# Kernel tuning notes

Hardware: AMD Instinct MI355X
Metric: run time of the kernel (lower is better)

Reference implementation:

```python
import jax, jax.numpy as jnp
import numpy as np

B, S, D = 2, 1024, 1024
N_HEADS = 16
R = 128
M = 8
N_NEURONS = 256


def group_gate(gate, n_basis):
    # gate: [B,S,N] -> [B,S,M], sum over consecutive groups, then normalize
    b, s, n = gate.shape
    gs = n // n_basis  # exact by construction (256/8)
    g = gate.reshape(b, s, n_basis, gs).sum(axis=-1)
    return g / (g.sum(axis=-1, keepdims=True) + 1e-8)


def feature_fn(x, neurons, weights):
    # x:[B,S,D], neurons:[M,D,R], weights:[B,S,M] -> h:[B,S,R]
    all_h = jnp.einsum('bsd,mdr->bsmr', x, neurons)
    return jnp.einsum('bsmr,bsm->bsr', all_h, weights)


def restore_fn(h, neurons, weights):
    # h:[B,S,R], neurons:[M,R,D], weights:[B,S,M] -> [B,S,D]
    pre = jnp.einsum('bsr,bsm->bsmr', h, weights)
    return jnp.einsum('bsmr,mrd->bsd', pre, neurons)


def setup_inputs() -> dict:
    key = jax.random.key(0)
    ks = jax.random.split(key, 9)
    sc = 0.02
    return {
        'x': jax.random.normal(ks[0], (B, S, D), jnp.float32),
        'qk_f': jax.random.normal(ks[1], (M, D, R), jnp.float32) * sc,
        'qk_r': jax.random.normal(ks[2], (M, R, D), jnp.float32) * sc,
        'v_f': jax.random.normal(ks[3], (M, D, R), jnp.float32) * sc,
        'v_r': jax.random.normal(ks[4], (M, R, D), jnp.float32) * sc,
        'Wg_q': jax.random.normal(ks[5], (D, N_NEURONS), jnp.float32) * sc,
        'Wg_k': jax.random.normal(ks[6], (D, N_NEURONS), jnp.float32) * sc,
        'Wg_v': jax.random.normal(ks[7], (D, N_NEURONS), jnp.float32) * sc,
        'W_O': jax.random.normal(ks[8], (D, D), jnp.float32) * sc,
    }


def reference(x, qk_f, qk_r, v_f, v_r, Wg_q, Wg_k, Wg_v, W_O):
    # Router gates (softmax over neuron dim), then grouped per basis
    g_Q = jax.nn.softmax(jnp.einsum('bsd,dn->bsn', x, Wg_q), axis=-1)
    g_K = jax.nn.softmax(jnp.einsum('bsd,dn->bsn', x, Wg_k), axis=-1)
    g_V = jax.nn.softmax(jnp.einsum('bsd,dn->bsn', x, Wg_v), axis=-1)
    gQ_b = group_gate(g_Q, M)
    gK_b = group_gate(g_K, M)
    gV_b = group_gate(g_V, M)

    Q = restore_fn(feature_fn(x, qk_f, gQ_b), qk_r, gQ_b)
    K = restore_fn(feature_fn(x, qk_f, gK_b), qk_r, gK_b)
    V = restore_fn(feature_fn(x, v_f, gV_b), v_r, gV_b)

    d_head = D // N_HEADS
    Q = Q.reshape(B, S, N_HEADS, d_head).transpose(0, 2, 1, 3)
    K = K.reshape(B, S, N_HEADS, d_head).transpose(0, 2, 1, 3)
    V = V.reshape(B, S, N_HEADS, d_head).transpose(0, 2, 1, 3)

    scale = jnp.sqrt(jnp.float32(d_head))
    scores = jnp.einsum('bhsd,bhtd->bhst', Q, K) / scale
    causal = jnp.tril(jnp.ones((S, S), dtype=jnp.bool_))
    scores = jnp.where(causal, scores, jnp.finfo(scores.dtype).min)
    attn_w = jax.nn.softmax(scores, axis=-1)
    out = jnp.einsum('bhst,bhtd->bhsd', attn_w, V)
    out = out.transpose(0, 2, 1, 3).reshape(B, S, D)
    out = jnp.einsum('bsd,de->bse', out, W_O)
    return out
```

## Files before the change

### kernel.cpp

```cpp
#include <hip/hip_runtime.h>
#include <hip/hip_bf16.h>

#define BB 2
#define SS 1024
#define DD 1024
#define NH 16
#define DH 64
#define MM 8
#define RR 128
#define NN 256
#define NT (BB*SS)

using bf16 = __hip_bfloat16;

typedef __attribute__((ext_vector_type(8))) short short8;
typedef __attribute__((ext_vector_type(4))) short short4v;
typedef __attribute__((ext_vector_type(4))) float f32x4;

#define EXP2F(x) __builtin_amdgcn_exp2f(x)

#define GLD16(g, l) __builtin_amdgcn_global_load_lds( \
    (const __attribute__((address_space(1))) void*)(g), \
    (__attribute__((address_space(3))) void*)(l), 16, 0, 0)

__device__ __forceinline__ short8 lds_load8(const short* p) {
    short4v a = *(const short4v*)p;
    short4v b = *(const short4v*)(p + 4);
    short8 r;
    r[0] = a[0]; r[1] = a[1]; r[2] = a[2]; r[3] = a[3];
    r[4] = b[0]; r[5] = b[1]; r[6] = b[2]; r[7] = b[3];
    return r;
}

template <int NR>
__device__ __forceinline__ void stage_tile(const bf16* __restrict__ src, int k0,
                                           bf16* lds, int wave, int lane) {
#pragma unroll
    for (int i = 0; i < NR / 32; ++i) {
        const int L = i * 256 + wave * 64 + lane;
        const int row = L >> 3;
        const int gch = (L & 7) ^ ((row >> 1) & 7);
        GLD16(src + (size_t)row * DD + k0 + gch * 8, &lds[(i * 256 + wave * 64) * 8]);
    }
}

__device__ __forceinline__ short8 fragld(const bf16* lds, int rc, int kk, int quad) {
    int slot = (kk * 4 + quad) ^ ((rc >> 1) & 7);
    return *(const short8*)&((const short*)lds)[(rc * 8 + slot) * 8];
}

__device__ __forceinline__ void gemm64_pipe2(
    const bf16* __restrict__ A, const bf16* __restrict__ Bt, bf16* __restrict__ C,
    int Nz, int m0, int n0, bf16* As, bf16* Bs,
    int wave, int lane, int quad, int l15) {
    const int wr = wave >> 1, wc = wave & 1;
    f32x4 acc[2][4];
#pragma unroll
    for (int i = 0; i < 2; ++i)
#pragma unroll
        for (int j = 0; j < 4; ++j) acc[i][j] = (f32x4)0.f;

    const bf16* Ab = A + (size_t)m0 * DD;
    const bf16* Bb = Bt + (size_t)n0 * DD;

    stage_tile<64>(Ab, 0, As, wave, lane);
    stage_tile<128>(Bb, 0, Bs, wave, lane);
    stage_tile<64>(Ab, 64, As + 4096, wave, lane);
    stage_tile<128>(Bb, 64, Bs + 8192, wave, lane);

    int cur = 0;
    for (int it = 0; it < 16; ++it) {
        const int k0 = it * 64;
        int nxt = cur + 2; if (nxt >= 3) nxt -= 3;
        if (it < 14) {
            stage_tile<64>(Ab, k0 + 128, As + nxt * 4096, wave, lane);
            stage_tile<128>(Bb, k0 + 128, Bs + nxt * 8192, wave, lane);
            asm volatile("s_waitcnt vmcnt(12)" ::: "memory");
        } else if (it == 14) {
            asm volatile("s_waitcnt vmcnt(6)" ::: "memory");
        } else {
            asm volatile("s_waitcnt vmcnt(0)" ::: "memory");
        }
        __builtin_amdgcn_s_barrier();

        const bf16* Asc = As + cur * 4096;
        const bf16* Bsc = Bs + cur * 8192;
#pragma unroll
        for (int kk = 0; kk < 2; ++kk) {
            short8 aF[2], bF[4];
#pragma unroll
            for (int bi = 0; bi < 2; ++bi) aF[bi] = fragld(Asc, wr * 32 + bi * 16 + l15, kk, quad);
#pragma unroll
            for (int bj = 0; bj < 4; ++bj) bF[bj] = fragld(Bsc, wc * 64 + bj * 16 + l15, kk, quad);
#pragma unroll
            for (int bi = 0; bi < 2; ++bi)
#pragma unroll
                for (int bj = 0; bj < 4; ++bj)
                    acc[bi][bj] = __builtin_amdgcn_mfma_f32_16x16x32_bf16(aF[bi], bF[bj], acc[bi][bj], 0, 0, 0);
        }
        __builtin_amdgcn_s_barrier();
        cur = cur + 1; if (cur == 3) cur = 0;
    }

#pragma unroll
    for (int bi = 0; bi < 2; ++bi)
#pragma unroll
        for (int bj = 0; bj < 4; ++bj)
#pragma unroll
            for (int r = 0; r < 4; ++r) {
                int row = m0 + wr * 32 + bi * 16 + quad * 4 + r;
                int col = n0 + wc * 64 + bj * 16 + l15;
                C[(size_t)row * Nz + col] = __float2bfloat16(acc[bi][bj][r]);
            }
}

struct ProjArgs {
    const bf16 *xb, *f0, *f1, *wg;
    bf16 *allh0, *allh1, *lg;
    const float* csrc[3];
    bf16* cdst[3];
};

__global__ __launch_bounds__(256, 2) void mfma_proj(ProjArgs P) {
    __shared__ __align__(16) char smem[73728];
    const int bidx = blockIdx.x;
    const int tid = threadIdx.x;

    if (bidx >= 704) {
        float (*tile)[33] = (float(*)[33])smem;
        const int cb = bidx - 704;
        const int j = cb >> 10;
        const int t = cb & 1023;
        const int kb = t >> 5, rb = t & 31;
        const int tx = tid & 31, ty0 = tid >> 5;
        const float* s = P.csrc[j] + ((size_t)(kb * 32) * 1024) + rb * 32 + tx;
#pragma unroll
        for (int p = 0; p < 4; ++p)
            tile[ty0 + p * 8][tx] = s[(size_t)(ty0 + p * 8) * 1024];
        __syncthreads();
        bf16* dd = P.cdst[j] + ((size_t)(rb * 32) * 1024) + kb * 32 + tx;
#pragma unroll
        for (int p = 0; p < 4; ++p)
            dd[(size_t)(ty0 + p * 8) * 1024] = __float2bfloat16(tile[tx][ty0 + p * 8]);
        return;
    }

    bf16* As = (bf16*)smem;
    bf16* Bs = As + 3 * 64 * 64;
    const int wave = tid >> 6, lane = tid & 63;
    const int quad = lane >> 4, l15 = lane & 15;
    const int wk = (bidx & 7) * 88 + (bidx >> 3);
    if (wk < 512) {
        const int z = wk >> 8;
        const int r = wk & 255;
        gemm64_pipe2(P.xb, z ? P.f1 : P.f0, z ? P.allh1 : P.allh0, 1024,
                     (r >> 3) * 64, (r & 7) * 128, As, Bs, wave, lane, quad, l15);
    } else {
        const int r = wk - 512;
        gemm64_pipe2(P.xb, P.wg, P.lg, 768, (r / 6) * 64, (r % 6) * 128,
                     As, Bs, wave, lane, quad, l15);
    }
}

struct RestZ {
    const bf16* A[3];
    const bf16* Bt[3];
    bf16* C[3];
};

__global__ __launch_bounds__(256, 2) void mfma_restore(RestZ R) {
    __shared__ __align__(16) char smem[73728];
    bf16* As = (bf16*)smem;
    bf16* Bs = As + 3 * 64 * 64;
    const int tid = threadIdx.x;
    const int wave = tid >> 6, lane = tid & 63;
    const int quad = lane >> 4, l15 = lane & 15;
    const int wk = (blockIdx.x & 7) * 96 + (blockIdx.x >> 3);
    const int z = wk >> 8;
    const int r = wk & 255;
    gemm64_pipe2(R.A[z], R.Bt[z], R.C[z], DD, (r >> 3) * 64, (r & 7) * 128,
                 As, Bs, wave, lane, quad, l15);
}

__global__ __launch_bounds__(256, 3) void mfma_wo(
    const bf16* __restrict__ A, const bf16* __restrict__ Bt, float* __restrict__ C) {
    __shared__ __align__(16) bf16 As[3 * 64 * 64];
    __shared__ __align__(16) bf16 Bs[3 * 64 * 64];
    const int tid = threadIdx.x;
    const int wave = tid >> 6, lane = tid & 63;
    const int quad = lane >> 4, l15 = lane & 15;
    const int wr = wave >> 1, wc = wave & 1;
    const int wk = (blockIdx.x & 7) * 64 + (blockIdx.x >> 3);
    const int m0 = (wk >> 4) * 64, n0 = (wk & 15) * 64;

    f32x4 acc[2][2];
#pragma unroll
    for (int i = 0; i < 2; ++i)
#pragma unroll
        for (int j = 0; j < 2; ++j) acc[i][j] = (f32x4)0.f;

    const bf16* Ab = A + (size_t)m0 * DD;
    const bf16* Bb = Bt + (size_t)n0 * DD;

    stage_tile<64>(Ab, 0, As, wave, lane);
    stage_tile<64>(Bb, 0, Bs, wave, lane);
    stage_tile<64>(Ab, 64, As + 4096, wave, lane);
    stage_tile<64>(Bb, 64, Bs + 4096, wave, lane);

    int cur = 0;
    for (int it = 0; it < 16; ++it) {
        const int k0 = it * 64;
        int nxt = cur + 2; if (nxt >= 3) nxt -= 3;
        if (it < 14) {
            stage_tile<64>(Ab, k0 + 128, As + nxt * 4096, wave, lane);
            stage_tile<64>(Bb, k0 + 128, Bs + nxt * 4096, wave, lane);
            asm volatile("s_waitcnt vmcnt(8)" ::: "memory");
        } else if (it == 14) {
            asm volatile("s_waitcnt vmcnt(4)" ::: "memory");
        } else {
            asm volatile("s_waitcnt vmcnt(0)" ::: "memory");
        }
        __builtin_amdgcn_s_barrier();

        const bf16* Asc = As + cur * 4096;
        const bf16* Bsc = Bs + cur * 4096;
#pragma unroll
        for (int kk = 0; kk < 2; ++kk) {
            short8 aF[2], bF[2];
#pragma unroll
            for (int bi = 0; bi < 2; ++bi) aF[bi] = fragld(Asc, wr * 32 + bi * 16 + l15, kk, quad);
#pragma unroll
            for (int bj = 0; bj < 2; ++bj) bF[bj] = fragld(Bsc, wc * 32 + bj * 16 + l15, kk, quad);
#pragma unroll
            for (int bi = 0; bi < 2; ++bi)
#pragma unroll
                for (int bj = 0; bj < 2; ++bj)
                    acc[bi][bj] = __builtin_amdgcn_mfma_f32_16x16x32_bf16(aF[bi], bF[bj], acc[bi][bj], 0, 0, 0);
        }
        __builtin_amdgcn_s_barrier();
        cur = cur + 1; if (cur == 3) cur = 0;
    }
#pragma unroll
    for (int bi = 0; bi < 2; ++bi)
#pragma unroll
        for (int bj = 0; bj < 2; ++bj)
#pragma unroll
            for (int r = 0; r < 4; ++r) {
                int row = m0 + wr * 32 + bi * 16 + quad * 4 + r;
                int col = n0 + wc * 32 + bj * 16 + l15;
                C[(size_t)row * DD + col] = acc[bi][bj][r];
            }
}

struct ConvJobs {
    const float* src[9];
    bf16* dst[9];
    int K[9], R[9], G[9];
    int tEnd[9];
};

__global__ void convert_kernel(ConvJobs J) {
    __shared__ float tile[32][33];
    const int b = blockIdx.x;
    int j = 0;
    while (j < 8 && b >= J.tEnd[j]) ++j;
    const int local = b - (j > 0 ? J.tEnd[j - 1] : 0);
    const float* src = J.src[j];
    bf16* dst = J.dst[j];
    const int tid = threadIdx.x;

    if (J.G[j] == 0) {
        size_t base = (size_t)local * 4096 + (size_t)tid * 16;
        const float4* s4 = (const float4*)(src + base);
        short* d = (short*)(dst + base);
#pragma unroll
        for (int c = 0; c < 4; ++c) {
            float4 v = s4[c];
            short4v o;
            bf16 t0 = __float2bfloat16(v.x); o[0] = *(short*)&t0;
            bf16 t1 = __float2bfloat16(v.y); o[1] = *(short*)&t1;
            bf16 t2 = __float2bfloat16(v.z); o[2] = *(short*)&t2;
            bf16 t3 = __float2bfloat16(v.w); o[3] = *(short*)&t3;
            *(short4v*)(d + c * 4) = o;
        }
    } else {
        const int Kj = J.K[j], Rj = J.R[j];
        const int Rb = Rj >> 5, Kb = Kj >> 5;
        const int perG = Kb * Rb;
        const int g = local / perG;
        const int rem = local - g * perG;
        const int kb = rem / Rb, rb = rem - kb * Rb;
        const int tx = tid & 31, ty0 = tid >> 5;
        const float* s = src + ((size_t)(g * Kj + kb * 32) * Rj) + rb * 32 + tx;
#pragma unroll
        for (int p = 0; p < 4; ++p)
            tile[ty0 + p * 8][tx] = s[(size_t)(ty0 + p * 8) * Rj];
        __syncthreads();
        bf16* dd = dst + ((size_t)(g * Rj + rb * 32) * Kj) + kb * 32 + tx;
#pragma unroll
        for (int p = 0; p < 4; ++p)
            dd[(size_t)(ty0 + p * 8) * Kj] = __float2bfloat16(tile[tx][ty0 + p * 8]);
    }
}

__global__ void gate_combine(const bf16* __restrict__ logitsAll,
                             const bf16* __restrict__ allh,
                             bf16* __restrict__ preQ, bf16* __restrict__ preK,
                             bf16* __restrict__ preV) {
    const int t = blockIdx.x;
    const int n = threadIdx.x;
    const int wave = n >> 6, lane = n & 63;
    __shared__ float wred[3][4];
    __shared__ float sred[3][4];
    __shared__ float gred[3][8];

    float v[3], e[3];
#pragma unroll
    for (int z = 0; z < 3; ++z)
        v[z] = __bfloat162float(logitsAll[(size_t)t * 768 + z * 256 + n]);

    float mz[3];
#pragma unroll
    for (int z = 0; z < 3; ++z) {
        mz[z] = v[z];
#pragma unroll
        for (int off = 1; off <= 32; off <<= 1)
            mz[z] = fmaxf(mz[z], __shfl_xor(mz[z], off));
    }
    if (lane == 0) {
#pragma unroll
        for (int z = 0; z < 3; ++z) wred[z][wave] = mz[z];
    }
    __syncthreads();
    float gmax[3];
#pragma unroll
    for (int z = 0; z < 3; ++z)
        gmax[z] = fmaxf(fmaxf(wred[z][0], wred[z][1]), fmaxf(wred[z][2], wred[z][3]));

    float ws[3];
#pragma unroll
    for (int z = 0; z < 3; ++z) {
        e[z] = __expf(v[z] - gmax[z]);
        ws[z] = e[z];
#pragma unroll
        for (int off = 1; off <= 32; off <<= 1)
            ws[z] += __shfl_xor(ws[z], off);
    }
    if (lane == 0) {
#pragma unroll
        for (int z = 0; z < 3; ++z) sred[z][wave] = ws[z];
    }
    float gs[3];
#pragma unroll
    for (int z = 0; z < 3; ++z) {
        gs[z] = e[z];
#pragma unroll
        for (int off = 1; off <= 16; off <<= 1)
            gs[z] += __shfl_xor(gs[z], off);
    }
    __syncthreads();
    float total[3];
#pragma unroll
    for (int z = 0; z < 3; ++z)
        total[z] = sred[z][0] + sred[z][1] + sred[z][2] + sred[z][3];
    if ((n & 31) == 0) {
#pragma unroll
        for (int z = 0; z < 3; ++z) gred[z][n >> 5] = gs[z] / total[z];
    }
    __syncthreads();

    float gv[3][8];
#pragma unroll
    for (int z = 0; z < 3; ++z) {
        float tot = 0.f;
#pragma unroll
        for (int m = 0; m < 8; ++m) tot += gred[z][m];
        float inv = 1.0f / (tot + 1e-8f);
#pragma unroll
        for (int m = 0; m < 8; ++m) gv[z][m] = gred[z][m] * inv;
    }

    const int r0 = n & 127;
    const int half = n >> 7;
    const bf16* src_qk = allh + (size_t)t * 1024;
    const bf16* src_v  = allh + (size_t)NT * DD + (size_t)t * 1024;
    float hq = 0.f, hk = 0.f, hv = 0.f;
#pragma unroll
    for (int m = 0; m < 8; ++m) {
        float aqk = __bfloat162float(src_qk[m * 128 + r0]);
        float av  = __bfloat162float(src_v[m * 128 + r0]);
        hq += aqk * gv[0][m];
        hk += aqk * gv[1][m];
        hv += av  * gv[2][m];
    }
    __syncthreads();
#pragma unroll
    for (int mm = 0; mm < 4; ++mm) {
        int m = half * 4 + mm;
        size_t o = (size_t)t * 1024 + m * 128 + r0;
        preQ[o] = __float2bfloat16(hq * gv[0][m]);
        preK[o] = __float2bfloat16(hk * gv[1][m]);
        preV[o] = __float2bfloat16(hv * gv[2][m]);
    }
}

#define LDK 68

__device__ const int FW24[24] = {
    62, 63, 60, 61, 14,
    58, 59, 56, 12,
    57, 54, 55, 52, 10,
    53, 50, 51, 48, 8,
    49, 6,
    4, 2, 0
};

__global__ __launch_bounds__(256) void flash_attn_hybrid(
    const bf16* __restrict__ Q, const bf16* __restrict__ K,
    const bf16* __restrict__ V, bf16* __restrict__ out,
    float* __restrict__ Opart, float* __restrict__ ml) {
    const int bx = blockIdx.x;
    const int e = FW24[bx >> 5];
    const int bh = bx & 31;
    const int split = e >> 5;
    const int qt = (e >> 1) & 15;
    const int half = e & 1;
    const int h0 = (qt + 2) >> 1;
    const int kt_lo = (split && half) ? h0 : 0;
    const int kt_hi = (split && !half) ? h0 : (qt + 1);
    const int b = bh >> 4;
    const int h = bh & 15;

    const int tid = threadIdx.x;
    const int wave = tid >> 6;
    const int lane = tid & 63;
    const int quad = lane >> 4;
    const int l15 = lane & 15;

    __shared__ short Ks[2][64 * 64];
    __shared__ short Vt[2][64 * LDK];
    __shared__ short Ps[4 * 16 * LDK];

    const int q_row = qt * 64 + wave * 16 + l15;
    const bf16* qptr = Q + (size_t)(b * SS + q_row) * DD + h * DH + quad * 8;
    short8 aq0 = *(const short8*)qptr;
    short8 aq1 = *(const short8*)(qptr + 32);

    const int krp = tid & 31;
    const int dhb = (tid >> 5) * 8;

    float m_r[4], l_r[4];
    f32x4 o[4];
#pragma unroll
    for (int r = 0; r < 4; ++r) { m_r[r] = -3.0e38f; l_r[r] = 0.f; }
#pragma unroll
    for (int cc = 0; cc < 4; ++cc) o[cc] = (f32x4)0.f;

    const float SCL2 = 0.18033688f;

    {
#pragma unroll
        for (int i = 0; i < 2; ++i) {
            const int L = i * 256 + wave * 64 + lane;
            const int row = L >> 3;
            const int gch = (L & 7) ^ ((row >> 1) & 7);
            GLD16(K + (size_t)(b * SS + kt_lo * 64 + row) * DD + h * DH + gch * 8,
                  &Ks[0][(i * 256 + wave * 64) * 8]);
        }
        const bf16* s0 = V + (size_t)(b * SS + kt_lo * 64 + 2 * krp) * DD + h * DH + dhb;
        short8 r0 = *(const short8*)s0;
        short8 r1 = *(const short8*)(s0 + DD);
#pragma unroll
        for (int i = 0; i < 8; ++i) {
            unsigned int pk = (unsigned short)r0[i] | ((unsigned int)(unsigned short)r1[i] << 16);
            *(unsigned int*)&Vt[0][(dhb + i) * LDK + 2 * krp] = pk;
        }
        __syncthreads();
    }

    for (int kt = kt_lo; kt < kt_hi; ++kt) {
        const int buf = (kt - kt_lo) & 1;
        const bool pf = (kt + 1 < kt_hi);
        short8 pr0, pr1;
        if (pf) {
#pragma unroll
            for (int i = 0; i < 2; ++i) {
                const int L = i * 256 + wave * 64 + lane;
                const int row = L >> 3;
                const int gch = (L & 7) ^ ((row >> 1) & 7);
                GLD16(K + (size_t)(b * SS + (kt + 1) * 64 + row) * DD + h * DH + gch * 8,
                      &Ks[buf ^ 1][(i * 256 + wave * 64) * 8]);
            }
            const bf16* s0 = V + (size_t)(b * SS + (kt + 1) * 64 + 2 * krp) * DD + h * DH + dhb;
            pr0 = *(const short8*)s0;
            pr1 = *(const short8*)(s0 + DD);
        }

        const short* KsB = Ks[buf];
        f32x4 s[4];
#pragma unroll
        for (int cc = 0; cc < 4; ++cc) {
            int n = cc * 16 + l15;
            int sl0 = quad ^ ((n >> 1) & 7);
            int sl1 = (quad + 4) ^ ((n >> 1) & 7);
            short8 bk0 = *(const short8*)&KsB[(n * 8 + sl0) * 8];
            short8 bk1 = *(const short8*)&KsB[(n * 8 + sl1) * 8];
            f32x4 acc = (f32x4)0.f;
            acc = __builtin_amdgcn_mfma_f32_16x16x32_bf16(aq0, bk0, acc, 0, 0, 0);
            acc = __builtin_amdgcn_mfma_f32_16x16x32_bf16(aq1, bk1, acc, 0, 0, 0);
            s[cc] = acc;
        }

        const bool diag = (kt == qt);
#pragma unroll
        for (int cc = 0; cc < 4; ++cc) {
#pragma unroll
            for (int r = 0; r < 4; ++r) {
                float v = s[cc][r] * SCL2;
                if (diag) {
                    int row_rel = wave * 16 + quad * 4 + r;
                    int col_rel = cc * 16 + l15;
                    if (col_rel > row_rel) v = -3.0e38f;
                }
                s[cc][r] = v;
            }
        }

        float mx[4];
#pragma unroll
        for (int r = 0; r < 4; ++r) {
            float m2 = fmaxf(fmaxf(s[0][r], s[1][r]), fmaxf(s[2][r], s[3][r]));
            m2 = fmaxf(m2, __shfl_xor(m2, 1));
            m2 = fmaxf(m2, __shfl_xor(m2, 2));
            m2 = fmaxf(m2, __shfl_xor(m2, 4));
            m2 = fmaxf(m2, __shfl_xor(m2, 8));
            mx[r] = m2;
        }
        bool grew = false;
#pragma unroll
        for (int r = 0; r < 4; ++r) grew = grew || (mx[r] > m_r[r] + 8.f);
        float alpha[4];
        const bool need = __any(grew);
        if (need) {
#pragma unroll
            for (int r = 0; r < 4; ++r) {
                float nm = fmaxf(m_r[r], mx[r]);
                alpha[r] = EXP2F(m_r[r] - nm);
                m_r[r] = nm;
            }
        }

        float p[4][4];
#pragma unroll
        for (int r = 0; r < 4; ++r) {
            float rs = 0.f;
#pragma unroll
            for (int cc = 0; cc < 4; ++cc) {
                float e2 = EXP2F(s[cc][r] - m_r[r]);
                p[cc][r] = e2;
                rs += e2;
            }
            rs += __shfl_xor(rs, 1);
            rs += __shfl_xor(rs, 2);
            rs += __shfl_xor(rs, 4);
            rs += __shfl_xor(rs, 8);
            if (need) l_r[r] = l_r[r] * alpha[r] + rs;
            else      l_r[r] += rs;
        }
        if (need) {
#pragma unroll
            for (int cc = 0; cc < 4; ++cc)
#pragma unroll
                for (int r = 0; r < 4; ++r) o[cc][r] *= alpha[r];
        }

        short* pw = &Ps[wave * 16 * LDK];
#pragma unroll
        for (int cc = 0; cc < 4; ++cc)
#pragma unroll
            for (int r = 0; r < 4; ++r) {
                bf16 hb = __float2bfloat16(p[cc][r]);
                pw[(quad * 4 + r) * LDK + cc * 16 + l15] = *(short*)&hb;
            }

        short8 ap0 = lds_load8(&pw[l15 * LDK + quad * 8]);
        short8 ap1 = lds_load8(&pw[l15 * LDK + 32 + quad * 8]);

        const short* VtB = Vt[buf];
#pragma unroll
        for (int cc = 0; cc < 4; ++cc) {
            short8 bv0 = lds_load8(&VtB[(cc * 16 + l15) * LDK + quad * 8]);
            short8 bv1 = lds_load8(&VtB[(cc * 16 + l15) * LDK + 32 + quad * 8]);
            o[cc] = __builtin_amdgcn_mfma_f32_16x16x32_bf16(ap0, bv0, o[cc], 0, 0, 0);
            o[cc] = __builtin_amdgcn_mfma_f32_16x16x32_bf16(ap1, bv1, o[cc], 0, 0, 0);
        }

        if (pf) {
#pragma unroll
            for (int i = 0; i < 8; ++i) {
                unsigned int pk = (unsigned short)pr0[i] | ((unsigned int)(unsigned short)pr1[i] << 16);
                *(unsigned int*)&Vt[buf ^ 1][(dhb + i) * LDK + 2 * krp] = pk;
            }
        }
        __syncthreads();
    }

    if (!split) {
        float inv[4];
#pragma unroll
        for (int r = 0; r < 4; ++r) inv[r] = 1.0f / l_r[r];
#pragma unroll
        for (int cc = 0; cc < 4; ++cc)
#pragma unroll
            for (int r = 0; r < 4; ++r) {
                int row = qt * 64 + wave * 16 + quad * 4 + r;
                out[(size_t)(b * SS + row) * DD + h * DH + cc * 16 + l15] =
                    __float2bfloat16(o[cc][r] * inv[r]);
            }
    } else {
        const int idx = (bh * 8 + (qt - 8)) * 2 + half;
        float* ob = Opart + (size_t)idx * 4096;
#pragma unroll
        for (int cc = 0; cc < 4; ++cc)
#pragma unroll
            for (int r = 0; r < 4; ++r) {
                int row = wave * 16 + quad * 4 + r;
                ob[row * 64 + cc * 16 + l15] = o[cc][r];
            }
        if (l15 == 0) {
#pragma unroll
            for (int r = 0; r < 4; ++r) {
                int row = wave * 16 + quad * 4 + r;
                ml[(size_t)idx * 128 + row] = m_r[r];
                ml[(size_t)idx * 128 + 64 + row] = l_r[r];
            }
        }
    }
}

__global__ void attn_combine(const float* __restrict__ Opart,
                             const float* __restrict__ ml,
                             bf16* __restrict__ out) {
    const int bidx = blockIdx.x;
    const int bh = bidx & 31;
    const int qt = (bidx >> 5) + 8;
    const int b = bh >> 4;
    const int h = bh & 15;
    const int tid = threadIdx.x;
    const int row = tid >> 2;
    const int cg = tid & 3;

    const int p0 = (bh * 8 + (qt - 8)) * 2;
    const int p1 = p0 + 1;
    float m0 = ml[(size_t)p0 * 128 + row], l0 = ml[(size_t)p0 * 128 + 64 + row];
    float m1 = ml[(size_t)p1 * 128 + row], l1 = ml[(size_t)p1 * 128 + 64 + row];
    float ms = fmaxf(m0, m1);
    float w0 = EXP2F(m0 - ms), w1 = EXP2F(m1 - ms);
    float inv = 1.0f / (l0 * w0 + l1 * w1);

    const float* o0 = Opart + (size_t)p0 * 4096 + row * 64 + cg * 16;
    const float* o1 = Opart + (size_t)p1 * 4096 + row * 64 + cg * 16;
    short out16[16];
#pragma unroll
    for (int j = 0; j < 16; j += 4) {
        float4 a = *(const float4*)(o0 + j);
        float4 bb = *(const float4*)(o1 + j);
        bf16 t0 = __float2bfloat16((a.x * w0 + bb.x * w1) * inv); out16[j] = *(short*)&t0;
        bf16 t1 = __float2bfloat16((a.y * w0 + bb.y * w1) * inv); out16[j + 1] = *(short*)&t1;
        bf16 t2 = __float2bfloat16((a.z * w0 + bb.z * w1) * inv); out16[j + 2] = *(short*)&t2;
        bf16 t3 = __float2bfloat16((a.w * w0 + bb.w * w1) * inv); out16[j + 3] = *(short*)&t3;
    }
    short* dst = (short*)(out + (size_t)(b * SS + qt * 64 + row) * DD + h * DH + cg * 16);
    *(short8*)dst = *(short8*)&out16[0];
    *(short8*)(dst + 8) = *(short8*)&out16[8];
}

extern "C" void kernel_launch(void* const* d_in, const int* in_sizes, int n_in,
                              void* d_out, int out_size, void* d_ws, size_t ws_size,
                              hipStream_t stream) {
    const float* x    = (const float*)d_in[0];
    const float* qk_f = (const float*)d_in[1];
    const float* qk_r = (const float*)d_in[2];
    const float* v_f  = (const float*)d_in[3];
    const float* v_r  = (const float*)d_in[4];
    const float* Wg_q = (const float*)d_in[5];
    const float* Wg_k = (const float*)d_in[6];
    const float* Wg_v = (const float*)d_in[7];
    const float* W_O  = (const float*)d_in[8];

    char* w = (char*)d_ws;
    const size_t MB = 1 << 20;
    bf16* xb     = (bf16*)(w + 0);
    bf16* wg_bt  = (bf16*)(w + 4 * MB);
    bf16* fbt    = (bf16*)(w + (size_t)(5.5 * MB));
    bf16* logits = (bf16*)(w + (size_t)(9.5 * MB));
    bf16* qkr_bt = (bf16*)(w + 16 * MB);
    bf16* vr_bt  = (bf16*)(w + 18 * MB);
    bf16* wo_bt  = (bf16*)(w + 20 * MB);
    bf16* preQ   = (bf16*)(w + 0);
    bf16* preK   = (bf16*)(w + 4 * MB);
    bf16* Kb     = (bf16*)(w + 8 * MB);
    bf16* Vb     = (bf16*)(w + 12 * MB);
    bf16* attnb  = (bf16*)(w + 0);
    float* Opart = (float*)(w + 32 * MB);
    float* mlbuf = (float*)(w + 48 * MB);
    bf16* allh   = (bf16*)d_out;
    bf16* preV   = allh + (size_t)NT * DD;
    bf16* Qb     = (bf16*)d_out;
    float* out   = (float*)d_out;

    ConvJobs J;
    J.src[0] = x;    J.dst[0] = xb;               J.K[0] = 0;    J.R[0] = 0;    J.G[0] = 0;
    J.src[1] = qk_f; J.dst[1] = fbt;              J.K[1] = 1024; J.R[1] = 128;  J.G[1] = 8;
    J.src[2] = v_f;  J.dst[2] = fbt + 1024*1024;  J.K[2] = 1024; J.R[2] = 128;  J.G[2] = 8;
    J.src[3] = Wg_q; J.dst[3] = wg_bt;            J.K[3] = 1024; J.R[3] = 256;  J.G[3] = 1;
    J.src[4] = Wg_k; J.dst[4] = wg_bt + 256*1024; J.K[4] = 1024; J.R[4] = 256;  J.G[4] = 1;
    J.src[5] = Wg_v; J.dst[5] = wg_bt + 2*256*1024; J.K[5] = 1024; J.R[5] = 256; J.G[5] = 1;
    int tiles[6] = {512, 1024, 1024, 256, 256, 256};
    int cum = 0;
    for (int i = 0; i < 6; ++i) { cum += tiles[i]; J.tEnd[i] = cum; }
    for (int i = 6; i < 9; ++i) { J.tEnd[i] = cum; J.src[i] = nullptr; J.dst[i] = nullptr; J.K[i] = J.R[i] = J.G[i] = 0; }
    convert_kernel<<<cum, 256, 0, stream>>>(J);

    ProjArgs Pp;
    Pp.xb = xb; Pp.f0 = fbt; Pp.f1 = fbt + 1024*1024; Pp.wg = wg_bt;
    Pp.allh0 = allh; Pp.allh1 = allh + (size_t)NT * DD; Pp.lg = logits;
    Pp.csrc[0] = qk_r; Pp.csrc[1] = v_r; Pp.csrc[2] = W_O;
    Pp.cdst[0] = qkr_bt; Pp.cdst[1] = vr_bt; Pp.cdst[2] = wo_bt;
    mfma_proj<<<dim3(3776), 256, 0, stream>>>(Pp);

    gate_combine<<<NT, 256, 0, stream>>>(logits, allh, preQ, preK, preV);

    RestZ Pr;
    Pr.A[0] = preQ; Pr.A[1] = preK; Pr.A[2] = preV;
    Pr.Bt[0] = qkr_bt; Pr.Bt[1] = qkr_bt; Pr.Bt[2] = vr_bt;
    Pr.C[0] = Qb; Pr.C[1] = Kb; Pr.C[2] = Vb;
    mfma_restore<<<dim3(768), 256, 0, stream>>>(Pr);

    flash_attn_hybrid<<<dim3(768), 256, 0, stream>>>(Qb, Kb, Vb, attnb, Opart, mlbuf);

    attn_combine<<<dim3(256), 256, 0, stream>>>(Opart, mlbuf, attnb);

    mfma_wo<<<dim3(512), 256, 0, stream>>>(attnb, wo_bt, out);
}
```

Before: 179.2 us.

## Enlarge projection and restore GEMM tiles to 128x128 with double buffering

```diff
diff --git a/kernel.cpp b/kernel.cpp
--- a/kernel.cpp
+++ b/kernel.cpp
@@ -49,66 +49,55 @@
     return *(const short8*)&((const short*)lds)[(rc * 8 + slot) * 8];
 }
 
-__device__ __forceinline__ void gemm64_pipe2(
+__device__ __forceinline__ void gemm128_pipe1(
     const bf16* __restrict__ A, const bf16* __restrict__ Bt, bf16* __restrict__ C,
     int Nz, int m0, int n0, bf16* As, bf16* Bs,
     int wave, int lane, int quad, int l15) {
     const int wr = wave >> 1, wc = wave & 1;
-    f32x4 acc[2][4];
-#pragma unroll
-    for (int i = 0; i < 2; ++i)
+    f32x4 acc[4][4];
+#pragma unroll
+    for (int i = 0; i < 4; ++i)
 #pragma unroll
         for (int j = 0; j < 4; ++j) acc[i][j] = (f32x4)0.f;
 
     const bf16* Ab = A + (size_t)m0 * DD;
     const bf16* Bb = Bt + (size_t)n0 * DD;
 
-    stage_tile<64>(Ab, 0, As, wave, lane);
+    stage_tile<128>(Ab, 0, As, wave, lane);
     stage_tile<128>(Bb, 0, Bs, wave, lane);
-    stage_tile<64>(Ab, 64, As + 4096, wave, lane);
-    stage_tile<128>(Bb, 64, Bs + 8192, wave, lane);
-
-    int cur = 0;
+    __syncthreads();
+
     for (int it = 0; it < 16; ++it) {
-        const int k0 = it * 64;
-        int nxt = cur + 2; if (nxt >= 3) nxt -= 3;
-        if (it < 14) {
-            stage_tile<64>(Ab, k0 + 128, As + nxt * 4096, wave, lane);
-            stage_tile<128>(Bb, k0 + 128, Bs + nxt * 8192, wave, lane);
-            asm volatile("s_waitcnt vmcnt(12)" ::: "memory");
-        } else if (it == 14) {
-            asm volatile("s_waitcnt vmcnt(6)" ::: "memory");
-        } else {
-            asm volatile("s_waitcnt vmcnt(0)" ::: "memory");
-        }
-        __builtin_amdgcn_s_barrier();
-
-        const bf16* Asc = As + cur * 4096;
-        const bf16* Bsc = Bs + cur * 8192;
+        const int buf = it & 1;
+        const bf16* Asc = As + buf * 8192;
+        const bf16* Bsc = Bs + buf * 8192;
+        if (it < 15) {
+            stage_tile<128>(Ab, (it + 1) * 64, As + (buf ^ 1) * 8192, wave, lane);
+            stage_tile<128>(Bb, (it + 1) * 64, Bs + (buf ^ 1) * 8192, wave, lane);
+        }
 #pragma unroll
         for (int kk = 0; kk < 2; ++kk) {
-            short8 aF[2], bF[4];
-#pragma unroll
-            for (int bi = 0; bi < 2; ++bi) aF[bi] = fragld(Asc, wr * 32 + bi * 16 + l15, kk, quad);
+            short8 aF[4], bF[4];
+#pragma unroll
+            for (int bi = 0; bi < 4; ++bi) aF[bi] = fragld(Asc, wr * 64 + bi * 16 + l15, kk, quad);
 #pragma unroll
             for (int bj = 0; bj < 4; ++bj) bF[bj] = fragld(Bsc, wc * 64 + bj * 16 + l15, kk, quad);
 #pragma unroll
-            for (int bi = 0; bi < 2; ++bi)
+            for (int bi = 0; bi < 4; ++bi)
 #pragma unroll
                 for (int bj = 0; bj < 4; ++bj)
                     acc[bi][bj] = __builtin_amdgcn_mfma_f32_16x16x32_bf16(aF[bi], bF[bj], acc[bi][bj], 0, 0, 0);
         }
-        __builtin_amdgcn_s_barrier();
-        cur = cur + 1; if (cur == 3) cur = 0;
-    }
-
-#pragma unroll
-    for (int bi = 0; bi < 2; ++bi)
+        __syncthreads();
+    }
+
+#pragma unroll
+    for (int bi = 0; bi < 4; ++bi)
 #pragma unroll
         for (int bj = 0; bj < 4; ++bj)
 #pragma unroll
             for (int r = 0; r < 4; ++r) {
-                int row = m0 + wr * 32 + bi * 16 + quad * 4 + r;
+                int row = m0 + wr * 64 + bi * 16 + quad * 4 + r;
                 int col = n0 + wc * 64 + bj * 16 + l15;
                 C[(size_t)row * Nz + col] = __float2bfloat16(acc[bi][bj][r]);
             }
@@ -122,13 +111,13 @@
 };
 
 __global__ __launch_bounds__(256, 2) void mfma_proj(ProjArgs P) {
-    __shared__ __align__(16) char smem[73728];
+    __shared__ __align__(16) char smem[65536];
     const int bidx = blockIdx.x;
     const int tid = threadIdx.x;
 
-    if (bidx >= 704) {
+    if (bidx >= 352) {
         float (*tile)[33] = (float(*)[33])smem;
-        const int cb = bidx - 704;
+        const int cb = bidx - 352;
         const int j = cb >> 10;
         const int t = cb & 1023;
         const int kb = t >> 5, rb = t & 31;
@@ -146,19 +135,19 @@
     }
 
     bf16* As = (bf16*)smem;
-    bf16* Bs = As + 3 * 64 * 64;
+    bf16* Bs = As + 2 * 128 * 64;
     const int wave = tid >> 6, lane = tid & 63;
     const int quad = lane >> 4, l15 = lane & 15;
-    const int wk = (bidx & 7) * 88 + (bidx >> 3);
-    if (wk < 512) {
-        const int z = wk >> 8;
-        const int r = wk & 255;
-        gemm64_pipe2(P.xb, z ? P.f1 : P.f0, z ? P.allh1 : P.allh0, 1024,
-                     (r >> 3) * 64, (r & 7) * 128, As, Bs, wave, lane, quad, l15);
+    const int wk = (bidx & 7) * 44 + (bidx >> 3);
+    if (wk < 256) {
+        const int z = wk >> 7;
+        const int r = wk & 127;
+        gemm128_pipe1(P.xb, z ? P.f1 : P.f0, z ? P.allh1 : P.allh0, 1024,
+                      (r >> 3) * 128, (r & 7) * 128, As, Bs, wave, lane, quad, l15);
     } else {
-        const int r = wk - 512;
-        gemm64_pipe2(P.xb, P.wg, P.lg, 768, (r / 6) * 64, (r % 6) * 128,
-                     As, Bs, wave, lane, quad, l15);
+        const int r = wk - 256;
+        gemm128_pipe1(P.xb, P.wg, P.lg, 768, (r / 6) * 128, (r % 6) * 128,
+                      As, Bs, wave, lane, quad, l15);
     }
 }
 
@@ -169,17 +158,17 @@
 };
 
 __global__ __launch_bounds__(256, 2) void mfma_restore(RestZ R) {
-    __shared__ __align__(16) char smem[73728];
+    __shared__ __align__(16) char smem[65536];
     bf16* As = (bf16*)smem;
-    bf16* Bs = As + 3 * 64 * 64;
+    bf16* Bs = As + 2 * 128 * 64;
     const int tid = threadIdx.x;
     const int wave = tid >> 6, lane = tid & 63;
     const int quad = lane >> 4, l15 = lane & 15;
-    const int wk = (blockIdx.x & 7) * 96 + (blockIdx.x >> 3);
-    const int z = wk >> 8;
-    const int r = wk & 255;
-    gemm64_pipe2(R.A[z], R.Bt[z], R.C[z], DD, (r >> 3) * 64, (r & 7) * 128,
-                 As, Bs, wave, lane, quad, l15);
+    const int wk = (blockIdx.x & 7) * 48 + (blockIdx.x >> 3);
+    const int z = wk >> 7;
+    const int r = wk & 127;
+    gemm128_pipe1(R.A[z], R.Bt[z], R.C[z], DD, (r >> 3) * 128, (r & 7) * 128,
+                  As, Bs, wave, lane, quad, l15);
 }
 
 __global__ __launch_bounds__(256, 3) void mfma_wo(
@@ -727,7 +716,7 @@
     Pp.allh0 = allh; Pp.allh1 = allh + (size_t)NT * DD; Pp.lg = logits;
     Pp.csrc[0] = qk_r; Pp.csrc[1] = v_r; Pp.csrc[2] = W_O;
     Pp.cdst[0] = qkr_bt; Pp.cdst[1] = vr_bt; Pp.cdst[2] = wo_bt;
-    mfma_proj<<<dim3(3776), 256, 0, stream>>>(Pp);
+    mfma_proj<<<dim3(3424), 256, 0, stream>>>(Pp);
 
     gate_combine<<<NT, 256, 0, stream>>>(logits, allh, preQ, preK, preV);
 
@@ -735,7 +724,7 @@
     Pr.A[0] = preQ; Pr.A[1] = preK; Pr.A[2] = preV;
     Pr.Bt[0] = qkr_bt; Pr.Bt[1] = qkr_bt; Pr.Bt[2] = vr_bt;
     Pr.C[0] = Qb; Pr.C[1] = Kb; Pr.C[2] = Vb;
-    mfma_restore<<<dim3(768), 256, 0, stream>>>(Pr);
+    mfma_restore<<<dim3(384), 256, 0, stream>>>(Pr);
 
     flash_attn_hybrid<<<dim3(768), 256, 0, stream>>>(Qb, Kb, Vb, attnb, Opart, mlbuf);
 
```

Result: faster. 172.9 us, median of 2 (-3.5%).
